# Kernel tuning notes

Measured on AMD Instinct MI355X. Metric: run time of the kernel, lower is better.

Reference implementation:

```python
import jax, jax.numpy as jnp
import numpy as np


def _apply_rope(x, cos, sin):
    # x: (..., T, D) with D even; cos/sin: (T, D), only even columns are used.
    x1, x2 = x[..., ::2], x[..., 1::2]
    c, s = cos[..., ::2], sin[..., ::2]
    even = x1 * c - x2 * s
    odd = x1 * s + x2 * c
    return jnp.stack((even, odd), axis=-1).reshape(x.shape)


def setup_inputs() -> dict:
    key = jax.random.key(0)
    B, T, C, H, G = 2, 2048, 4096, 32, 4  # batch, seq, n_embd, n_head, n_query_groups
    Dh = C // H            # 128
    n_kv = H // G          # 8 kv heads
    ks = jax.random.split(key, 5)
    w = 0.02
    x = jax.random.normal(ks[0], (B, T, C), jnp.float32)
    wq = jax.random.normal(ks[1], (C, H * Dh), jnp.float32) * w
    wk = jax.random.normal(ks[2], (C, n_kv * Dh), jnp.float32) * w
    wv = jax.random.normal(ks[3], (C, n_kv * Dh), jnp.float32) * w
    wo = jax.random.normal(ks[4], (C, C), jnp.float32) * w
    inv_freq = 1.0 / (10000.0 ** (jnp.arange(0, Dh, 2, dtype=jnp.float32) / Dh))
    ang = jnp.arange(T, dtype=jnp.float32)[:, None] * inv_freq[None, :]  # (T, Dh/2)
    cos = jnp.repeat(jnp.cos(ang), 2, axis=-1)  # (T, Dh)
    sin = jnp.repeat(jnp.sin(ang), 2, axis=-1)
    return {"x": x, "wq": wq, "wk": wk, "wv": wv, "wo": wo, "cos": cos, "sin": sin, "is_causal": 1}


def reference(x, wq, wk, wv, wo, cos, sin, is_causal):
    B, T, C = x.shape
    Dh = cos.shape[-1]
    H = wq.shape[1] // Dh
    n_kv = wk.shape[1] // Dh
    G = H // n_kv  # query-group repeat factor
    scale = 1.0 / jnp.sqrt(jnp.float32(Dh))

    q = (x @ wq).reshape(B, T, H, Dh).transpose(0, 2, 1, 3)      # (B,H,T,Dh)
    k = (x @ wk).reshape(B, T, n_kv, Dh).transpose(0, 2, 1, 3)   # (B,nkv,T,Dh)
    v = (x @ wv).reshape(B, T, n_kv, Dh).transpose(0, 2, 1, 3)

    c, s = cos[:T], sin[:T]
    q = _apply_rope(q, c, s)
    k = _apply_rope(k, c, s)

    # GQA without materializing repeated K/V: q head h attends kv head h // G
    # (matches repeat_interleave ordering: kv head j duplicated to q heads j*G..j*G+G-1)
    qg = q.reshape(B, n_kv, G, T, Dh)
    scores = jnp.einsum("bkgtd,bksd->bkgts", qg, k) * scale       # (B,nkv,G,T,T)
    if is_causal:
        mask = jnp.tril(jnp.ones((T, T), dtype=bool))
        scores = jnp.where(mask, scores, jnp.finfo(scores.dtype).min)
    attn = jax.nn.softmax(scores, axis=-1)
    out = jnp.einsum("bkgts,bksd->bkgtd", attn, v)                # (B,nkv,G,T,Dh)
    out = out.reshape(B, H, T, Dh).transpose(0, 2, 1, 3).reshape(B, T, C)
    return out @ wo
```

## Files before the change

kernel.cpp:

```cpp
#include <hip/hip_runtime.h>
#include <hip/hip_bf16.h>

#define BSZ   2
#define TSEQ  2048
#define CDIM  4096
#define NH    32
#define NKV   8
#define GQ    4
#define DH    128
#define BT    (BSZ * TSEQ)

typedef short   bf16x8  __attribute__((ext_vector_type(8)));
typedef float   f32x4   __attribute__((ext_vector_type(4)));
typedef unsigned short ushort8v __attribute__((ext_vector_type(8)));
typedef unsigned short u16;

#define LDS_AS(p) ((__attribute__((address_space(3))) void*)(p))
#define GLB_AS(p) ((const __attribute__((address_space(1))) void*)(p))

static __device__ inline unsigned short bf16_bits(float f) {
  __hip_bfloat16 h = __float2bfloat16(f);
  return *(unsigned short*)&h;
}
static __device__ inline float bits_f32(unsigned short u) {
  unsigned v = ((unsigned)u) << 16;
  return __builtin_bit_cast(float, v);
}

__global__ __launch_bounds__(256) void cvt_bf16x4(
    const float* __restrict__ src, __hip_bfloat16* __restrict__ dst, int n4) {
  int i = blockIdx.x * 256 + threadIdx.x;
  if (i >= n4) return;
  float4 v = ((const float4*)src)[i];
  ushort4 o;
  o.x = bf16_bits(v.x); o.y = bf16_bits(v.y);
  o.z = bf16_bits(v.z); o.w = bf16_bits(v.w);
  ((ushort4*)dst)[i] = o;
}

__global__ __launch_bounds__(256) void transpose_cvt(
    const float* __restrict__ src, __hip_bfloat16* __restrict__ dst, int K, int N) {
  __shared__ float T[64][65];
  const int bn = blockIdx.x * 64;
  const int bk = blockIdx.y * 64;
  const int tid = threadIdx.x;
  for (int i = tid; i < 64 * 16; i += 256) {
    int r = i >> 4, c4 = i & 15;
    float4 v = *(const float4*)&src[(size_t)(bk + r) * N + bn + c4 * 4];
    T[r][c4*4+0] = v.x; T[r][c4*4+1] = v.y; T[r][c4*4+2] = v.z; T[r][c4*4+3] = v.w;
  }
  __syncthreads();
  for (int i = tid; i < 64 * 16; i += 256) {
    int n = i >> 4, k4 = i & 15;
    ushort4 o;
    o.x = bf16_bits(T[k4*4+0][n]); o.y = bf16_bits(T[k4*4+1][n]);
    o.z = bf16_bits(T[k4*4+2][n]); o.w = bf16_bits(T[k4*4+3][n]);
    *(ushort4*)&dst[(size_t)(bn + n) * K + bk + k4 * 4] = o;
  }
}

__global__ __launch_bounds__(256) void gemm_mfma(
    const __hip_bfloat16* __restrict__ A, const __hip_bfloat16* __restrict__ Bt,
    void* __restrict__ C, int N, int K, int outBf16) {
  __shared__ __hip_bfloat16 As[128 * 32];
  __shared__ __hip_bfloat16 Bs[128 * 32];
  const int tid  = threadIdx.x;
  const int lane = tid & 63;
  const int wv   = tid >> 6;
  const int row0 = blockIdx.y * 128;
  const int col0 = blockIdx.x * 128;
  const int wm   = (wv & 1) * 64;
  const int wn   = (wv >> 1) * 64;
  const int lrow = lane & 15;
  const int kgrp = lane >> 4;

  f32x4 zero = {0.f, 0.f, 0.f, 0.f};
  f32x4 acc[4][4];
  #pragma unroll
  for (int mi = 0; mi < 4; ++mi)
    #pragma unroll
    for (int ni = 0; ni < 4; ++ni) acc[mi][ni] = zero;

  for (int k0 = 0; k0 < K; k0 += 32) {
    #pragma unroll
    for (int r = 0; r < 2; ++r) {
      int idx16 = r * 256 + tid;
      int arow  = idx16 >> 2;
      int akk   = (idx16 & 3) << 3;
      const __hip_bfloat16* ga = &A [(size_t)(row0 + arow) * K + k0 + akk];
      const __hip_bfloat16* gb = &Bt[(size_t)(col0 + arow) * K + k0 + akk];
      char* la = (char*)As + (r * 4096 + wv * 1024 + lane * 16);
      char* lb = (char*)Bs + (r * 4096 + wv * 1024 + lane * 16);
      __builtin_amdgcn_global_load_lds(GLB_AS(ga), LDS_AS(la), 16, 0, 0);
      __builtin_amdgcn_global_load_lds(GLB_AS(gb), LDS_AS(lb), 16, 0, 0);
    }
    __syncthreads();
    bf16x8 af[4], bfr[4];
    #pragma unroll
    for (int i = 0; i < 4; ++i) {
      af[i]  = *(const bf16x8*)&As[(wm + i * 16 + lrow) * 32 + kgrp * 8];
      bfr[i] = *(const bf16x8*)&Bs[(wn + i * 16 + lrow) * 32 + kgrp * 8];
    }
    #pragma unroll
    for (int mi = 0; mi < 4; ++mi)
      #pragma unroll
      for (int ni = 0; ni < 4; ++ni)
        acc[mi][ni] = __builtin_amdgcn_mfma_f32_16x16x32_bf16(af[mi], bfr[ni], acc[mi][ni], 0, 0, 0);
    __syncthreads();
  }

  if (outBf16) {
    __hip_bfloat16* Cb = (__hip_bfloat16*)C;
    #pragma unroll
    for (int mi = 0; mi < 4; ++mi)
      #pragma unroll
      for (int ni = 0; ni < 4; ++ni) {
        int col = col0 + wn + ni * 16 + lrow;
        int rowb = row0 + wm + mi * 16 + kgrp * 4;
        #pragma unroll
        for (int r = 0; r < 4; ++r)
          Cb[(size_t)(rowb + r) * N + col] = __float2bfloat16(acc[mi][ni][r]);
      }
  } else {
    float* Cf = (float*)C;
    #pragma unroll
    for (int mi = 0; mi < 4; ++mi)
      #pragma unroll
      for (int ni = 0; ni < 4; ++ni) {
        int col = col0 + wn + ni * 16 + lrow;
        int rowb = row0 + wm + mi * 16 + kgrp * 4;
        #pragma unroll
        for (int r = 0; r < 4; ++r)
          Cf[(size_t)(rowb + r) * N + col] = acc[mi][ni][r];
      }
  }
}

__global__ __launch_bounds__(512, 2) void gemm256(
    const __hip_bfloat16* __restrict__ A, const __hip_bfloat16* __restrict__ Bt,
    void* __restrict__ C, int N, int K, int outBf16) {
  __shared__ __hip_bfloat16 AsBuf[2][16384];
  __shared__ __hip_bfloat16 BsBuf[2][16384];

  const int tid  = threadIdx.x;
  const int lane = tid & 63;
  const int wid  = tid >> 6;
  const int wm   = wid >> 2;
  const int wn   = wid & 3;
  const int quad = lane >> 4;
  const int l15  = lane & 15;

  const int nbx = N >> 8;
  int bid = blockIdx.y * nbx + blockIdx.x;
  const int nwg = nbx * (int)gridDim.y;
  if ((nwg & 7) == 0) bid = (bid & 7) * (nwg >> 3) + (bid >> 3);
  const int row0 = (bid / nbx) << 8;
  const int col0 = (bid % nbx) << 8;

  const int NT = K >> 6;

  const int xr  = (l15 & 7) << 4;
  const int ke0 = (((quad * 16)      ^ xr) >> 1);
  const int ke1 = (((64 + quad * 16) ^ xr) >> 1);
  const int arE = (wm * 128 + l15) * 64;
  const int brE = (wn * 64  + l15) * 64;

#define STG(srcp, r0g, ldsb, h, k0e) do {                                          \
    _Pragma("unroll")                                                              \
    for (int j = 0; j < 2; ++j) {                                                  \
      int p    = (j * 512 + tid) << 4;                      \
      int prow = p >> 7;                                                           \
      int koff = (p & 127) ^ ((prow & 7) << 4);                                    \
      const __hip_bfloat16* gsrc =                                                 \
          (srcp) + (size_t)((r0g) + (h) * 128 + prow) * K + (k0e) + (koff >> 1);   \
      char* ldst = (char*)(ldsb) + (h) * 16384 + p;                                \
      __builtin_amdgcn_global_load_lds(GLB_AS(gsrc), LDS_AS(ldst), 16, 0, 0);      \
    }                                                                              \
  } while (0)

  f32x4 acc[8][4];
  #pragma unroll
  for (int i = 0; i < 8; ++i)
    #pragma unroll
    for (int j = 0; j < 4; ++j) acc[i][j] = (f32x4){0.f, 0.f, 0.f, 0.f};

  STG(A,  row0, &AsBuf[0][0], 0, 0);
  STG(A,  row0, &AsBuf[0][0], 1, 0);
  STG(Bt, col0, &BsBuf[0][0], 0, 0);
  STG(Bt, col0, &BsBuf[0][0], 1, 0);
  if (NT > 1) {
    STG(Bt, col0, &BsBuf[1][0], 0, 64);
    STG(Bt, col0, &BsBuf[1][0], 1, 64);
    asm volatile("s_waitcnt vmcnt(4)" ::: "memory");
  } else {
    asm volatile("s_waitcnt vmcnt(0)" ::: "memory");
  }
  __builtin_amdgcn_s_barrier();

  for (int t = 0; t < NT; ++t) {
    const int d  = t & 1, od = d ^ 1;
    char* Aod = (char*)&AsBuf[od][0];
    char* Bd  = (char*)&BsBuf[d][0];
    const int k1 = (t + 1) << 6, k2 = (t + 2) << 6;
    bf16x8 aH[4][2], b0[2][2], b1[2][2];

    #pragma unroll
    for (int m = 0; m < 4; ++m) {
      aH[m][0] = *(const bf16x8*)&AsBuf[d][arE + m * 1024 + ke0];
      aH[m][1] = *(const bf16x8*)&AsBuf[d][arE + m * 1024 + ke1];
    }
    #pragma unroll
    for (int n = 0; n < 2; ++n) {
      b0[n][0] = *(const bf16x8*)&BsBuf[d][brE + n * 1024 + ke0];
      b0[n][1] = *(const bf16x8*)&BsBuf[d][brE + n * 1024 + ke1];
    }
    if (t + 1 < NT) STG(A, row0, Aod, 0, k1);
    __builtin_amdgcn_s_barrier();
    asm volatile("s_waitcnt lgkmcnt(0)" ::: "memory");
    __builtin_amdgcn_s_setprio(1);
    #pragma unroll
    for (int m = 0; m < 4; ++m)
      #pragma unroll
      for (int n = 0; n < 2; ++n) {
        acc[m][n] = __builtin_amdgcn_mfma_f32_16x16x32_bf16(aH[m][0], b0[n][0], acc[m][n], 0, 0, 0);
        acc[m][n] = __builtin_amdgcn_mfma_f32_16x16x32_bf16(aH[m][1], b0[n][1], acc[m][n], 0, 0, 0);
      }
    __builtin_amdgcn_s_setprio(0);
    __builtin_amdgcn_s_barrier();

    #pragma unroll
    for (int n = 0; n < 2; ++n) {
      b1[n][0] = *(const bf16x8*)&BsBuf[d][brE + (n + 2) * 1024 + ke0];
      b1[n][1] = *(const bf16x8*)&BsBuf[d][brE + (n + 2) * 1024 + ke1];
    }
    if (t + 1 < NT) STG(A, row0, Aod, 1, k1);
    __builtin_amdgcn_s_barrier();
    asm volatile("s_waitcnt lgkmcnt(0)" ::: "memory");
    __builtin_amdgcn_s_setprio(1);
    #pragma unroll
    for (int m = 0; m < 4; ++m)
      #pragma unroll
      for (int n = 0; n < 2; ++n) {
        acc[m][n + 2] = __builtin_amdgcn_mfma_f32_16x16x32_bf16(aH[m][0], b1[n][0], acc[m][n + 2], 0, 0, 0);
        acc[m][n + 2] = __builtin_amdgcn_mfma_f32_16x16x32_bf16(aH[m][1], b1[n][1], acc[m][n + 2], 0, 0, 0);
      }
    __builtin_amdgcn_s_setprio(0);
    __builtin_amdgcn_s_barrier();

    #pragma unroll
    for (int m = 0; m < 4; ++m) {
      aH[m][0] = *(const bf16x8*)&AsBuf[d][arE + 4096 + m * 1024 + ke0];
      aH[m][1] = *(const bf16x8*)&AsBuf[d][arE + 4096 + m * 1024 + ke1];
    }
    if (t + 2 < NT) STG(Bt, col0, Bd, 0, k2);
    __builtin_amdgcn_s_barrier();
    asm volatile("s_waitcnt lgkmcnt(0)" ::: "memory");
    __builtin_amdgcn_s_setprio(1);
    #pragma unroll
    for (int m = 0; m < 4; ++m)
      #pragma unroll
      for (int n = 0; n < 2; ++n) {
        acc[m + 4][n + 2] = __builtin_amdgcn_mfma_f32_16x16x32_bf16(aH[m][0], b1[n][0], acc[m + 4][n + 2], 0, 0, 0);
        acc[m + 4][n + 2] = __builtin_amdgcn_mfma_f32_16x16x32_bf16(aH[m][1], b1[n][1], acc[m + 4][n + 2], 0, 0, 0);
      }
    __builtin_amdgcn_s_setprio(0);
    __builtin_amdgcn_s_barrier();

    if (t + 2 < NT) STG(Bt, col0, Bd, 1, k2);
    __builtin_amdgcn_s_barrier();
    __builtin_amdgcn_s_setprio(1);
    #pragma unroll
    for (int m = 0; m < 4; ++m)
      #pragma unroll
      for (int n = 0; n < 2; ++n) {
        acc[m + 4][n] = __builtin_amdgcn_mfma_f32_16x16x32_bf16(aH[m][0], b0[n][0], acc[m + 4][n], 0, 0, 0);
        acc[m + 4][n] = __builtin_amdgcn_mfma_f32_16x16x32_bf16(aH[m][1], b0[n][1], acc[m + 4][n], 0, 0, 0);
      }
    __builtin_amdgcn_s_setprio(0);
    if (t < NT - 2)       asm volatile("s_waitcnt vmcnt(4)" ::: "memory");
    else if (t == NT - 2) asm volatile("s_waitcnt vmcnt(0)" ::: "memory");
    __builtin_amdgcn_s_barrier();
  }
#undef STG

  if (outBf16) {
    __hip_bfloat16* Cb = (__hip_bfloat16*)C;
    #pragma unroll
    for (int mi = 0; mi < 8; ++mi)
      #pragma unroll
      for (int ni = 0; ni < 4; ++ni) {
        int col  = col0 + wn * 64 + ni * 16 + l15;
        int rowb = row0 + wm * 128 + mi * 16 + quad * 4;
        #pragma unroll
        for (int r = 0; r < 4; ++r)
          Cb[(size_t)(rowb + r) * N + col] = __float2bfloat16(acc[mi][ni][r]);
      }
  } else {
    float* Cf = (float*)C;
    #pragma unroll
    for (int mi = 0; mi < 8; ++mi)
      #pragma unroll
      for (int ni = 0; ni < 4; ++ni) {
        int col  = col0 + wn * 64 + ni * 16 + l15;
        int rowb = row0 + wm * 128 + mi * 16 + quad * 4;
        #pragma unroll
        for (int r = 0; r < 4; ++r)
          Cf[(size_t)(rowb + r) * N + col] = acc[mi][ni][r];
      }
  }
}

__global__ __launch_bounds__(256) void rope_bf16(
    __hip_bfloat16* __restrict__ buf, int stride, int perRow,
    const float* __restrict__ cosb, const float* __restrict__ sinb) {
  int idx = blockIdx.x * 256 + threadIdx.x;
  int row = idx / perRow;
  if (row >= BT) return;
  int c8 = (idx - row * perRow) * 8;
  int t  = row & (TSEQ - 1);
  int cp = c8 & (DH - 1);
  __hip_bfloat16* p = buf + (size_t)row * stride + c8;
  ushort8v raw = *(const ushort8v*)p;
  const float* cr = &cosb[(size_t)t * DH + cp];
  const float* sr = &sinb[(size_t)t * DH + cp];
  ushort8v outp;
  #pragma unroll
  for (int j = 0; j < 8; j += 2) {
    float x1 = bits_f32(raw[j]), x2 = bits_f32(raw[j + 1]);
    float c = cr[j], s = sr[j];
    outp[j]     = bf16_bits(x1 * c - x2 * s);
    outp[j + 1] = bf16_bits(x1 * s + x2 * c);
  }
  *(ushort8v*)p = outp;
}

__global__ __launch_bounds__(256) void transpose_v(
    const __hip_bfloat16* __restrict__ kvsrc, u16* __restrict__ vt) {
  __shared__ u16 T[64][72];
  const int tid  = threadIdx.x;
  const int tile = blockIdx.x, kvh = blockIdx.y, b = blockIdx.z;
  u16* dst = vt + ((size_t)((b * NKV + kvh) * 32 + tile)) * (128 * 64);
  for (int half = 0; half < 2; ++half) {
    #pragma unroll
    for (int it = 0; it < 2; ++it) {
      int idx = it * 256 + tid;
      int r = idx >> 3, c8 = idx & 7;
      ushort8v vdat = *(const ushort8v*)&kvsrc[
          (size_t)(b * TSEQ + tile * 64 + r) * 2048 + 1024 + kvh * DH + half * 64 + c8 * 8];
      *(ushort8v*)&T[r][c8 * 8] = vdat;
    }
    __syncthreads();
    #pragma unroll
    for (int it = 0; it < 2; ++it) {
      int idx = it * 256 + tid;
      int d = idx >> 3, c8 = idx & 7;
      ushort8v o8;
      #pragma unroll
      for (int j = 0; j < 8; ++j) o8[j] = T[c8 * 8 + j][d];
      *(ushort8v*)&dst[(size_t)(half * 64 + d) * 64 + c8 * 8] = o8;
    }
    __syncthreads();
  }
}

#define KSTR 130
#define VSTR 66
#define PSTR 68

__global__ __launch_bounds__(256) void flash_mfma(
    const __hip_bfloat16* __restrict__ q,
    const __hip_bfloat16* __restrict__ kv,
    const u16* __restrict__ vt,
    __hip_bfloat16* __restrict__ o,
    const int* __restrict__ causal_p) {
  __shared__ u16 Ks[64 * KSTR];
  __shared__ u16 Vs[128 * VSTR];
  __shared__ u16 Ps[4][16 * PSTR];

  const int tid  = threadIdx.x;
  const int lane = tid & 63;
  const int wq   = tid >> 6;
  const int quad = lane >> 4;
  const int l15  = lane & 15;
  const int mtile = blockIdx.x, h = blockIdx.y, b = blockIdx.z;
  const int kvh = h >> 2;
  const int m0  = mtile * 64;
  const bool causal = (*causal_p != 0);
  const float NEG_INF = -__builtin_inff();
  const float scale = 0.08838834764831845f;

  bf16x8 qf[4];
  {
    const __hip_bfloat16* qrow =
        &q[(size_t)(b * TSEQ + m0 + wq * 16 + l15) * CDIM + h * DH + quad * 8];
    #pragma unroll
    for (int kc = 0; kc < 4; ++kc) qf[kc] = *(const bf16x8*)(qrow + kc * 32);
  }

  f32x4 Ot[8];
  #pragma unroll
  for (int dt = 0; dt < 8; ++dt) Ot[dt] = (f32x4){0.f, 0.f, 0.f, 0.f};
  float mrow[4] = {NEG_INF, NEG_INF, NEG_INF, NEG_INF};
  float lrow[4] = {0.f, 0.f, 0.f, 0.f};

  const int ntiles = causal ? (mtile + 1) : (TSEQ / 64);
  u16* Pw = &Ps[wq][0];

  for (int tile = 0; tile < ntiles; ++tile) {
    const int j0 = tile * 64;
    __syncthreads();
    #pragma unroll
    for (int it = 0; it < 4; ++it) {
      int idx = it * 256 + tid;
      int r = idx >> 4, c8 = idx & 15;
      ushort8v kd = *(const ushort8v*)&kv[(size_t)(b * TSEQ + j0 + r) * 2048 + kvh * DH + c8 * 8];
      *(ushort8v*)&Ks[r * KSTR + c8 * 8] = kd;
    }
    const u16* vblob = vt + ((size_t)((b * NKV + kvh) * 32 + tile)) * (128 * 64);
    #pragma unroll
    for (int it = 0; it < 4; ++it) {
      int idx = it * 256 + tid;
      int d = idx >> 3, c8 = idx & 7;
      ushort8v vd = *(const ushort8v*)&vblob[(size_t)d * 64 + c8 * 8];
      *(ushort8v*)&Vs[d * VSTR + c8 * 8] = vd;
    }
    __syncthreads();

    f32x4 S[4];
    #pragma unroll
    for (int jt = 0; jt < 4; ++jt) {
      f32x4 acc = {0.f, 0.f, 0.f, 0.f};
      #pragma unroll
      for (int kc = 0; kc < 4; ++kc) {
        bf16x8 kf = *(const bf16x8*)&Ks[(jt * 16 + l15) * KSTR + kc * 32 + quad * 8];
        acc = __builtin_amdgcn_mfma_f32_16x16x32_bf16(qf[kc], kf, acc, 0, 0, 0);
      }
      S[jt] = acc;
    }
    #pragma unroll
    for (int jt = 0; jt < 4; ++jt)
      #pragma unroll
      for (int r = 0; r < 4; ++r) S[jt][r] *= scale;
    if (causal && tile == mtile) {
      const int qr0 = m0 + wq * 16 + quad * 4;
      #pragma unroll
      for (int jt = 0; jt < 4; ++jt)
        #pragma unroll
        for (int r = 0; r < 4; ++r)
          if (j0 + jt * 16 + l15 > qr0 + r) S[jt][r] = NEG_INF;
    }

    float rmax[4], alpha[4], rsum[4];
    #pragma unroll
    for (int r = 0; r < 4; ++r) {
      float mx = fmaxf(fmaxf(S[0][r], S[1][r]), fmaxf(S[2][r], S[3][r]));
      #pragma unroll
      for (int w = 1; w <= 8; w <<= 1) mx = fmaxf(mx, __shfl_xor(mx, w));
      rmax[r] = mx;
      float mn = fmaxf(mrow[r], mx);
      alpha[r] = __expf(mrow[r] - mn);
      mrow[r] = mn;
      rsum[r] = 0.f;
    }
    #pragma unroll
    for (int jt = 0; jt < 4; ++jt)
      #pragma unroll
      for (int r = 0; r < 4; ++r) {
        float p = __expf(S[jt][r] - mrow[r]);
        rsum[r] += p;
        Pw[(quad * 4 + r) * PSTR + jt * 16 + l15] = bf16_bits(p);
      }
    #pragma unroll
    for (int r = 0; r < 4; ++r) {
      float s = rsum[r];
      #pragma unroll
      for (int w = 1; w <= 8; w <<= 1) s += __shfl_xor(s, w);
      lrow[r] = lrow[r] * alpha[r] + s;
    }
    #pragma unroll
    for (int dt = 0; dt < 8; ++dt)
      #pragma unroll
      for (int r = 0; r < 4; ++r) Ot[dt][r] *= alpha[r];

    #pragma unroll
    for (int kc = 0; kc < 2; ++kc) {
      bf16x8 pf = *(const bf16x8*)&Pw[l15 * PSTR + kc * 32 + quad * 8];
      #pragma unroll
      for (int dt = 0; dt < 8; ++dt) {
        bf16x8 vf = *(const bf16x8*)&Vs[(dt * 16 + l15) * VSTR + kc * 32 + quad * 8];
        Ot[dt] = __builtin_amdgcn_mfma_f32_16x16x32_bf16(pf, vf, Ot[dt], 0, 0, 0);
      }
    }
  }

  float invl[4];
  #pragma unroll
  for (int r = 0; r < 4; ++r) invl[r] = 1.f / lrow[r];
  #pragma unroll
  for (int dt = 0; dt < 8; ++dt)
    #pragma unroll
    for (int r = 0; r < 4; ++r)
      o[(size_t)(b * TSEQ + m0 + wq * 16 + quad * 4 + r) * CDIM + h * DH + dt * 16 + l15] =
          __float2bfloat16(Ot[dt][r] * invl[r]);
}

extern "C" void kernel_launch(void* const* d_in, const int* in_sizes, int n_in,
                              void* d_out, int out_size, void* d_ws, size_t ws_size,
                              hipStream_t stream) {
  const float* x    = (const float*)d_in[0];
  const float* wq   = (const float*)d_in[1];
  const float* wk   = (const float*)d_in[2];
  const float* wv   = (const float*)d_in[3];
  const float* wo   = (const float*)d_in[4];
  const float* cosb = (const float*)d_in[5];
  const float* sinb = (const float*)d_in[6];
  const int* causal = (const int*)d_in[7];

  char* wsb = (char*)d_ws;
  __hip_bfloat16* xb   = (__hip_bfloat16*)(wsb);
  __hip_bfloat16* woT  = (__hip_bfloat16*)(wsb);
  __hip_bfloat16* wqT  = (__hip_bfloat16*)(wsb + (((size_t)32) << 20));
  __hip_bfloat16* obuf = (__hip_bfloat16*)(wsb + (((size_t)32) << 20));
  __hip_bfloat16* wkvT = (__hip_bfloat16*)(wsb + (((size_t)64) << 20));
  u16*            vtb  = (u16*)           (wsb + (((size_t)64) << 20));
  __hip_bfloat16* kvb  = (__hip_bfloat16*)(wsb + (((size_t)80) << 20));
  __hip_bfloat16* qb   = (__hip_bfloat16*)d_out;

  dim3 blk(256);
  dim3 blk5(512);
  cvt_bf16x4<<<dim3((BT * CDIM / 4 + 255) / 256), blk, 0, stream>>>(x, xb, BT * CDIM / 4);
  transpose_cvt<<<dim3(CDIM / 64, CDIM / 64), blk, 0, stream>>>(wq, wqT, CDIM, CDIM);
  transpose_cvt<<<dim3(1024 / 64, CDIM / 64), blk, 0, stream>>>(wk, wkvT, CDIM, 1024);
  transpose_cvt<<<dim3(1024 / 64, CDIM / 64), blk, 0, stream>>>(wv, wkvT + (size_t)1024 * CDIM, CDIM, 1024);
  gemm256<<<dim3(CDIM / 256, BT / 256), blk5, 0, stream>>>(xb, wqT, qb, CDIM, CDIM, 1);
  gemm_mfma<<<dim3(2048 / 128, BT / 128), blk, 0, stream>>>(xb, wkvT, kvb, 2048, CDIM, 1);
  transpose_v<<<dim3(32, NKV, BSZ), blk, 0, stream>>>(kvb, vtb);
  rope_bf16<<<dim3(BT * (CDIM / 8) / 256), blk, 0, stream>>>(qb, CDIM, CDIM / 8, cosb, sinb);
  rope_bf16<<<dim3(BT * (1024 / 8) / 256), blk, 0, stream>>>(kvb, 2048, 1024 / 8, cosb, sinb);
  transpose_cvt<<<dim3(CDIM / 64, CDIM / 64), blk, 0, stream>>>(wo, woT, CDIM, CDIM);
  flash_mfma<<<dim3(TSEQ / 64, NH, BSZ), blk, 0, stream>>>(qb, kvb, vtb, obuf, causal);
  gemm256<<<dim3(CDIM / 256, BT / 256), blk5, 0, stream>>>(obuf, woT, d_out, CDIM, CDIM, 0);
}
```

Before: 1.102 ms.

## Prefetch next K/V tile into registers and XOR-swizzle LDS layout in flash kernel

The flash attention kernel now loads the next K and V tiles from global memory into registers while the current tile's QK and PV MFMAs run, then writes them to LDS after compute. Separately, the padded LDS strides are replaced with an XOR swizzle on 8-element chunks to avoid bank conflicts without padding. The aim is to hide global load latency behind compute and make LDS reads conflict-free. In exchange it adds register pressure and keeps two barriers per tile. The LDS stores remain serialized after compute.

```diff
diff --git a/kernel.cpp b/kernel.cpp
--- a/kernel.cpp
+++ b/kernel.cpp
@@ -363,8 +363,6 @@
   }
 }
 
-#define KSTR 130
-#define VSTR 66
 #define PSTR 68
 
 __global__ __launch_bounds__(256) void flash_mfma(
@@ -373,8 +371,8 @@
     const u16* __restrict__ vt,
     __hip_bfloat16* __restrict__ o,
     const int* __restrict__ causal_p) {
-  __shared__ u16 Ks[64 * KSTR];
-  __shared__ u16 Vs[128 * VSTR];
+  __shared__ u16 Ks[64 * 128];
+  __shared__ u16 Vs[128 * 64];
   __shared__ u16 Ps[4][16 * PSTR];
 
   const int tid  = threadIdx.x;
@@ -388,6 +386,7 @@
   const bool causal = (*causal_p != 0);
   const float NEG_INF = -__builtin_inff();
   const float scale = 0.08838834764831845f;
+  const int swz = (l15 & 7) << 3;
 
   bf16x8 qf[4];
   {
@@ -405,26 +404,40 @@
 
   const int ntiles = causal ? (mtile + 1) : (TSEQ / 64);
   u16* Pw = &Ps[wq][0];
+  const u16* vtbase = vt + ((size_t)(b * NKV + kvh) * 32) * (128 * 64);
+
+  ushort8v kreg[4], vreg[4];
+  #pragma unroll
+  for (int it = 0; it < 4; ++it) {
+    int idx = it * 256 + tid;
+    int r = idx >> 4, c8 = idx & 15;
+    kreg[it] = *(const ushort8v*)&kv[(size_t)(b * TSEQ + r) * 2048 + kvh * DH + c8 * 8];
+    int d = idx >> 3, c8v = idx & 7;
+    vreg[it] = *(const ushort8v*)&vtbase[(size_t)d * 64 + c8v * 8];
+  }
+  #pragma unroll
+  for (int it = 0; it < 4; ++it) {
+    int idx = it * 256 + tid;
+    int r = idx >> 4, c8 = idx & 15;
+    *(ushort8v*)&Ks[r * 128 + ((c8 ^ (r & 7)) * 8)] = kreg[it];
+    int d = idx >> 3, c8v = idx & 7;
+    *(ushort8v*)&Vs[d * 64 + ((c8v ^ (d & 7)) * 8)] = vreg[it];
+  }
+  __syncthreads();
 
   for (int tile = 0; tile < ntiles; ++tile) {
     const int j0 = tile * 64;
-    __syncthreads();
-    #pragma unroll
-    for (int it = 0; it < 4; ++it) {
-      int idx = it * 256 + tid;
-      int r = idx >> 4, c8 = idx & 15;
-      ushort8v kd = *(const ushort8v*)&kv[(size_t)(b * TSEQ + j0 + r) * 2048 + kvh * DH + c8 * 8];
-      *(ushort8v*)&Ks[r * KSTR + c8 * 8] = kd;
-    }
-    const u16* vblob = vt + ((size_t)((b * NKV + kvh) * 32 + tile)) * (128 * 64);
-    #pragma unroll
-    for (int it = 0; it < 4; ++it) {
-      int idx = it * 256 + tid;
-      int d = idx >> 3, c8 = idx & 7;
-      ushort8v vd = *(const ushort8v*)&vblob[(size_t)d * 64 + c8 * 8];
-      *(ushort8v*)&Vs[d * VSTR + c8 * 8] = vd;
-    }
-    __syncthreads();
+    if (tile + 1 < ntiles) {
+      const u16* vblob = vtbase + (size_t)(tile + 1) * (128 * 64);
+      #pragma unroll
+      for (int it = 0; it < 4; ++it) {
+        int idx = it * 256 + tid;
+        int r = idx >> 4, c8 = idx & 15;
+        kreg[it] = *(const ushort8v*)&kv[(size_t)(b * TSEQ + j0 + 64 + r) * 2048 + kvh * DH + c8 * 8];
+        int d = idx >> 3, c8v = idx & 7;
+        vreg[it] = *(const ushort8v*)&vblob[(size_t)d * 64 + c8v * 8];
+      }
+    }
 
     f32x4 S[4];
     #pragma unroll
@@ -432,7 +445,7 @@
       f32x4 acc = {0.f, 0.f, 0.f, 0.f};
       #pragma unroll
       for (int kc = 0; kc < 4; ++kc) {
-        bf16x8 kf = *(const bf16x8*)&Ks[(jt * 16 + l15) * KSTR + kc * 32 + quad * 8];
+        bf16x8 kf = *(const bf16x8*)&Ks[(jt * 16 + l15) * 128 + ((kc * 32 + quad * 8) ^ swz)];
         acc = __builtin_amdgcn_mfma_f32_16x16x32_bf16(qf[kc], kf, acc, 0, 0, 0);
       }
       S[jt] = acc;
@@ -450,13 +463,12 @@
           if (j0 + jt * 16 + l15 > qr0 + r) S[jt][r] = NEG_INF;
     }
 
-    float rmax[4], alpha[4], rsum[4];
+    float alpha[4], rsum[4];
     #pragma unroll
     for (int r = 0; r < 4; ++r) {
       float mx = fmaxf(fmaxf(S[0][r], S[1][r]), fmaxf(S[2][r], S[3][r]));
       #pragma unroll
       for (int w = 1; w <= 8; w <<= 1) mx = fmaxf(mx, __shfl_xor(mx, w));
-      rmax[r] = mx;
       float mn = fmaxf(mrow[r], mx);
       alpha[r] = __expf(mrow[r] - mn);
       mrow[r] = mn;
@@ -487,9 +499,22 @@
       bf16x8 pf = *(const bf16x8*)&Pw[l15 * PSTR + kc * 32 + quad * 8];
       #pragma unroll
       for (int dt = 0; dt < 8; ++dt) {
-        bf16x8 vf = *(const bf16x8*)&Vs[(dt * 16 + l15) * VSTR + kc * 32 + quad * 8];
+        bf16x8 vf = *(const bf16x8*)&Vs[(dt * 16 + l15) * 64 + ((kc * 32 + quad * 8) ^ swz)];
         Ot[dt] = __builtin_amdgcn_mfma_f32_16x16x32_bf16(pf, vf, Ot[dt], 0, 0, 0);
       }
+    }
+
+    if (tile + 1 < ntiles) {
+      __syncthreads();
+      #pragma unroll
+      for (int it = 0; it < 4; ++it) {
+        int idx = it * 256 + tid;
+        int r = idx >> 4, c8 = idx & 15;
+        *(ushort8v*)&Ks[r * 128 + ((c8 ^ (r & 7)) * 8)] = kreg[it];
+        int d = idx >> 3, c8v = idx & 7;
+        *(ushort8v*)&Vs[d * 64 + ((c8v ^ (d & 7)) * 8)] = vreg[it];
+      }
+      __syncthreads();
     }
   }
 
```

Measured after the change: 1.008 ms. 1.09x faster.
